# Performance work log

Measured on AMD Instinct MI355X. Metric: run time of the kernel, lower is better.

Reference implementation:

```python
import jax, jax.numpy as jnp
import numpy as np

B, NG, NM, E, K, D = 1, 65536, 8192, 262144, 32, 128
EPS = 1e-5


def layernorm(x, g, b):
    mu = jnp.mean(x, axis=-1, keepdims=True)
    var = jnp.mean(jnp.square(x - mu), axis=-1, keepdims=True)
    return (x - mu) * jax.lax.rsqrt(var + EPS) * g + b


def mlp(x, W, g, b):
    # Linear (no bias) -> tanh -> LayerNorm, matching MLP module
    return layernorm(jnp.tanh(x @ W), g, b)


def setup_inputs() -> dict:
    key = jax.random.key(0)
    ks = jax.random.split(key, 16)
    inp = {
        "grid_mesh_bond_embedding": jax.random.normal(ks[0], (B, E, D), jnp.float32),
        "grid_rect_embedding": jax.random.normal(ks[1], (B, NG, D), jnp.float32),
        "mesh_node_embedding": jax.random.normal(ks[2], (B, NM, D), jnp.float32),
        "edge_id2pair": jnp.stack(
            [jax.random.randint(ks[3], (E,), 0, NG),
             jax.random.randint(ks[4], (E,), 0, NM)], axis=1),  # [E,2] int
        "edge_id_of_node": jax.random.randint(ks[5], (NM, K), 0, E),  # [NM,K] int
        "edge_coef": jax.random.uniform(ks[6], (NM, K, 1), jnp.float32),
        # MLP_G2M_GM2E: Linear(3D -> D), LayerNorm(D)
        "W_gm2e": jax.random.normal(ks[7], (3 * D, D), jnp.float32) / np.sqrt(3 * D),
        "g_gm2e": jnp.ones((D,), jnp.float32),
        "b_gm2e": jnp.zeros((D,), jnp.float32),
        # MLP_G2M_E2M: Linear(2D -> D), LayerNorm(D)
        "W_e2m": jax.random.normal(ks[8], (2 * D, D), jnp.float32) / np.sqrt(2 * D),
        "g_e2m": jnp.ones((D,), jnp.float32),
        "b_e2m": jnp.zeros((D,), jnp.float32),
        # MLP_G2M_G2G: Linear(D -> D), LayerNorm(D)
        "W_g2g": jax.random.normal(ks[9], (D, D), jnp.float32) / np.sqrt(D),
        "g_g2g": jnp.ones((D,), jnp.float32),
        "b_g2g": jnp.zeros((D,), jnp.float32),
    }
    return inp


def reference(grid_mesh_bond_embedding, grid_rect_embedding, mesh_node_embedding,
              edge_id2pair, edge_id_of_node, edge_coef,
              W_gm2e, g_gm2e, b_gm2e, W_e2m, g_e2m, b_e2m, W_g2g, g_g2g, b_g2g):
    # Edge update: gather rect/node endpoints, concat, MLP -> [B,E,D]
    rect_src = grid_rect_embedding[:, edge_id2pair[:, 0]]  # [B,E,D]
    node_dst = mesh_node_embedding[:, edge_id2pair[:, 1]]  # [B,E,D]
    edge_in = jnp.concatenate([grid_mesh_bond_embedding, rect_src, node_dst], axis=-1)
    delta_edge = mlp(edge_in, W_gm2e, g_gm2e, b_gm2e)  # [B,E,D]

    # Node update: gather K edges per mesh node, coef-weighted mean over K
    gathered = delta_edge[:, edge_id_of_node]  # [B,NM,K,D]
    agg = jnp.mean(gathered * edge_coef, axis=-2)  # [B,NM,D]
    delta_node = mlp(jnp.concatenate([mesh_node_embedding, agg], axis=-1), W_e2m, g_e2m, b_e2m)

    # Grid rect self-update
    delta_rect = mlp(grid_rect_embedding, W_g2g, g_g2g, b_g2g)

    return (grid_mesh_bond_embedding + delta_edge,
            grid_rect_embedding + delta_rect,
            mesh_node_embedding + delta_node)
```

## Files before the change

kernel.cpp:

```cpp
#include <hip/hip_runtime.h>


typedef __bf16 bf16x8 __attribute__((ext_vector_type(8)));
typedef __bf16 bf16x4 __attribute__((ext_vector_type(4)));
typedef float f32x4 __attribute__((ext_vector_type(4)));
typedef unsigned int u32x4 __attribute__((ext_vector_type(4)));

#define E_CNT 262144
#define NG_CNT 65536
#define NM_CNT 8192

#define WF_A 0
#define WF_B 16384
#define WF_C 32768
#define WF_3 49152
#define WF_2 65536
#define WF_TOT 98304

__device__ __forceinline__ float fast_tanh(float x) {
  float e = __expf(2.f * x);
  return 1.f - 2.f / (1.f + e);
}

__global__ __launch_bounds__(256) void convert_w_kernel(
    const float* __restrict__ W1, const float* __restrict__ W2,
    const float* __restrict__ W3, __bf16* __restrict__ WF) {
  const int cid = blockIdx.x * 256 + threadIdx.x;
  if (cid >= 12288) return;
  const float* src;
  __bf16* dst;
  int local;
  if (cid < 2048) { src = W1; local = cid; dst = WF + WF_A; }
  else if (cid < 4096) { src = W1 + 128 * 128; local = cid - 2048; dst = WF + WF_B; }
  else if (cid < 6144) { src = W1 + 256 * 128; local = cid - 4096; dst = WF + WF_C; }
  else if (cid < 8192) { src = W3; local = cid - 6144; dst = WF + WF_3; }
  else { src = W2; local = cid - 8192; dst = WF + WF_2; }
  const int lane6 = local & 63, cx = lane6 & 15, qq = lane6 >> 4;
  const int kkn = local >> 6, kk = kkn >> 3, nn = kkn & 7;
  const int k0 = kk * 32 + qq * 8, col = nn * 16 + cx;
  bf16x8 v;
#pragma unroll
  for (int j = 0; j < 8; ++j) v[j] = (__bf16)src[(k0 + j) * 128 + col];
  *(bf16x8*)(dst + local * 8) = v;
}

__device__ __forceinline__ void stage_copy(const __bf16* __restrict__ wf,
                                           __bf16* wt, int nelems) {
  const int n16 = nelems >> 3;
  for (int i = threadIdx.x; i < n16; i += blockDim.x)
    *(u32x4*)(wt + i * 8) = *(const u32x4*)(wf + i * 8);
}

template <bool STORE_D>
__device__ __forceinline__ void mlp_epilogue(f32x4* acc, const f32x4* R,
                                             const float* gvec,
                                             const float* bvec, int q,
                                             float* op, __bf16* dp) {
  float s1 = 0.f, s2 = 0.f;
#pragma unroll
  for (int n = 0; n < 8; ++n)
#pragma unroll
    for (int j = 0; j < 4; ++j) {
      float v = fast_tanh(acc[n][j]);
      acc[n][j] = v;
      s1 += v;
      s2 += v * v;
    }
  s1 += __shfl_xor(s1, 16, 64);
  s2 += __shfl_xor(s2, 16, 64);
  s1 += __shfl_xor(s1, 32, 64);
  s2 += __shfl_xor(s2, 32, 64);
  const float mu = s1 * (1.f / 128.f);
  const float rs = rsqrtf(s2 * (1.f / 128.f) - mu * mu + 1e-5f);
#pragma unroll
  for (int n = 0; n < 8; ++n) {
    const f32x4 G = *(const f32x4*)(gvec + n * 16 + q * 4);
    const f32x4 Bv = *(const f32x4*)(bvec + n * 16 + q * 4);
    f32x4 o;
    bf16x4 db;
#pragma unroll
    for (int j = 0; j < 4; ++j) {
      const float d = (acc[n][j] - mu) * rs * G[j] + Bv[j];
      o[j] = R[n][j] + d;
      db[j] = (__bf16)d;
    }
    *(f32x4*)(op + n * 16 + q * 4) = o;
    if (STORE_D) *(bf16x4*)(dp + n * 16 + q * 4) = db;
  }
}

template <bool STORE_D>
__global__ __launch_bounds__(256, 3) void edge_kernel(
    const float* __restrict__ gm, const int* __restrict__ pair,
    const __bf16* __restrict__ P1, const __bf16* __restrict__ P2,
    const __bf16* __restrict__ WF, const float* __restrict__ gvec,
    const float* __restrict__ bvec, float* __restrict__ out,
    __bf16* __restrict__ delta_out) {
  __shared__ __bf16 wt[16384];
  stage_copy(WF, wt, 16384);
  __syncthreads();
  const int tid = threadIdx.x, lane = tid & 63, wid = tid >> 6;
  const int r = lane & 15, q = lane >> 4;
  const __bf16* wl = wt + lane * 8;
  const int row = ((blockIdx.x * 4 + wid) << 4) + r;

  const int2 sd = *(const int2*)(pair + 2 * (size_t)row);
  const float* pa = gm + (size_t)row * 128;
  f32x4 F[4][2];
#pragma unroll
  for (int kk = 0; kk < 4; ++kk) {
    F[kk][0] = *(const f32x4*)(pa + kk * 32 + q * 8);
    F[kk][1] = *(const f32x4*)(pa + kk * 32 + q * 8 + 4);
  }
  bf16x4 pg1[8], pg2[8];
  {
    const __bf16* p1 = P1 + (size_t)sd.x * 128 + q * 4;
    const __bf16* p2 = P2 + (size_t)sd.y * 128 + q * 4;
#pragma unroll
    for (int n = 0; n < 8; ++n) {
      pg1[n] = *(const bf16x4*)(p1 + n * 16);
      pg2[n] = *(const bf16x4*)(p2 + n * 16);
    }
  }
  f32x4 R[8];
#pragma unroll
  for (int n = 0; n < 8; ++n) R[n] = *(const f32x4*)(pa + n * 16 + q * 4);

  bf16x8 ab[4];
#pragma unroll
  for (int kk = 0; kk < 4; ++kk)
#pragma unroll
    for (int j = 0; j < 4; ++j) {
      ab[kk][j] = (__bf16)F[kk][0][j];
      ab[kk][4 + j] = (__bf16)F[kk][1][j];
    }
  f32x4 acc[8] = {};
#pragma unroll
  for (int kk = 0; kk < 4; ++kk)
#pragma unroll
    for (int n = 0; n < 8; ++n)
      acc[n] = __builtin_amdgcn_mfma_f32_16x16x32_bf16(
          *(const bf16x8*)(wl + (kk * 8 + n) * 512), ab[kk], acc[n], 0, 0, 0);
#pragma unroll
  for (int n = 0; n < 8; ++n)
#pragma unroll
    for (int j = 0; j < 4; ++j)
      acc[n][j] += (float)pg1[n][j] + (float)pg2[n][j];

  mlp_epilogue<STORE_D>(acc, R, gvec, bvec, q, out + (size_t)row * 128,
                        STORE_D ? delta_out + (size_t)row * 128 : nullptr);
}

__global__ __launch_bounds__(256) void rect_fused_kernel(
    const float* __restrict__ rect, const __bf16* __restrict__ WFb,
    const __bf16* __restrict__ WF3, const float* __restrict__ gvec,
    const float* __restrict__ bvec, float* __restrict__ out1,
    __bf16* __restrict__ P1) {
  __shared__ __bf16 wt[32768];
  stage_copy(WFb, wt, 16384);
  stage_copy(WF3, wt + 16384, 16384);
  __syncthreads();
  const int tid = threadIdx.x, lane = tid & 63, wid = tid >> 6;
  const int r = lane & 15, q = lane >> 4;
  const __bf16* wl = wt + lane * 8;
  const int row0 = ((blockIdx.x * 8 + wid) << 4) + r;
#pragma unroll 1
  for (int half = 0; half < 2; ++half) {
    const int row = row0 + half * 64;
    const float* pa = rect + (size_t)row * 128;
    f32x4 F[4][2];
#pragma unroll
    for (int kk = 0; kk < 4; ++kk) {
      F[kk][0] = *(const f32x4*)(pa + kk * 32 + q * 8);
      F[kk][1] = *(const f32x4*)(pa + kk * 32 + q * 8 + 4);
    }
    bf16x8 ab[4];
#pragma unroll
    for (int kk = 0; kk < 4; ++kk)
#pragma unroll
      for (int j = 0; j < 4; ++j) {
        ab[kk][j] = (__bf16)F[kk][0][j];
        ab[kk][4 + j] = (__bf16)F[kk][1][j];
      }
    f32x4 acc[8] = {};
#pragma unroll
    for (int kk = 0; kk < 4; ++kk)
#pragma unroll
      for (int n = 0; n < 8; ++n)
        acc[n] = __builtin_amdgcn_mfma_f32_16x16x32_bf16(
            *(const bf16x8*)(wl + (kk * 8 + n) * 512), ab[kk], acc[n], 0, 0, 0);
    __bf16* pp = P1 + (size_t)row * 128;
#pragma unroll
    for (int n = 0; n < 8; ++n) {
      bf16x4 o;
#pragma unroll
      for (int j = 0; j < 4; ++j) o[j] = (__bf16)acc[n][j];
      *(bf16x4*)(pp + n * 16 + q * 4) = o;
    }
    f32x4 acc2[8] = {};
#pragma unroll
    for (int kk = 0; kk < 4; ++kk)
#pragma unroll
      for (int n = 0; n < 8; ++n)
        acc2[n] = __builtin_amdgcn_mfma_f32_16x16x32_bf16(
            *(const bf16x8*)(wl + 16384 + (kk * 8 + n) * 512), ab[kk], acc2[n],
            0, 0, 0);
    f32x4 R[8];
#pragma unroll
    for (int n = 0; n < 8; ++n) R[n] = *(const f32x4*)(pa + n * 16 + q * 4);
    mlp_epilogue<false>(acc2, R, gvec, bvec, q, out1 + (size_t)row * 128,
                        nullptr);
  }
}

__global__ __launch_bounds__(256) void mlp128_kernel(
    const float* __restrict__ A, const __bf16* __restrict__ WFx,
    const float* __restrict__ gvec, const float* __restrict__ bvec,
    float* __restrict__ out, int M) {
  __shared__ __bf16 wt[16384];
  stage_copy(WFx, wt, 16384);
  __syncthreads();
  const int tid = threadIdx.x, lane = tid & 63, wid = tid >> 6;
  const int r = lane & 15, q = lane >> 4;
  const __bf16* wl = wt + lane * 8;
  const int t = blockIdx.x * 4 + wid;
  if (t >= (M >> 4)) return;
  const int row = (t << 4) + r;
  const float* pa = A + (size_t)row * 128;
  f32x4 F[4][2];
#pragma unroll
  for (int kk = 0; kk < 4; ++kk) {
    F[kk][0] = *(const f32x4*)(pa + kk * 32 + q * 8);
    F[kk][1] = *(const f32x4*)(pa + kk * 32 + q * 8 + 4);
  }
  bf16x8 ab[4];
#pragma unroll
  for (int kk = 0; kk < 4; ++kk)
#pragma unroll
    for (int j = 0; j < 4; ++j) {
      ab[kk][j] = (__bf16)F[kk][0][j];
      ab[kk][4 + j] = (__bf16)F[kk][1][j];
    }
  f32x4 acc[8] = {};
#pragma unroll
  for (int kk = 0; kk < 4; ++kk)
#pragma unroll
    for (int n = 0; n < 8; ++n)
      acc[n] = __builtin_amdgcn_mfma_f32_16x16x32_bf16(
          *(const bf16x8*)(wl + (kk * 8 + n) * 512), ab[kk], acc[n], 0, 0, 0);
  f32x4 R[8];
#pragma unroll
  for (int n = 0; n < 8; ++n) R[n] = *(const f32x4*)(pa + n * 16 + q * 4);
  mlp_epilogue<false>(acc, R, gvec, bvec, q, out + (size_t)row * 128, nullptr);
}

__global__ __launch_bounds__(256) void lin_kernel(
    const float* __restrict__ A, const __bf16* __restrict__ WFx,
    __bf16* __restrict__ out, int M) {
  __shared__ __bf16 wt[16384];
  stage_copy(WFx, wt, 16384);
  __syncthreads();
  const int tid = threadIdx.x, lane = tid & 63, wid = tid >> 6;
  const int r = lane & 15, q = lane >> 4;
  const __bf16* wl = wt + lane * 8;
  const int t = blockIdx.x * 4 + wid;
  if (t >= (M >> 4)) return;
  const int row = (t << 4) + r;
  const float* pa = A + (size_t)row * 128;
  f32x4 F[4][2];
#pragma unroll
  for (int kk = 0; kk < 4; ++kk) {
    F[kk][0] = *(const f32x4*)(pa + kk * 32 + q * 8);
    F[kk][1] = *(const f32x4*)(pa + kk * 32 + q * 8 + 4);
  }
  bf16x8 ab[4];
#pragma unroll
  for (int kk = 0; kk < 4; ++kk)
#pragma unroll
    for (int j = 0; j < 4; ++j) {
      ab[kk][j] = (__bf16)F[kk][0][j];
      ab[kk][4 + j] = (__bf16)F[kk][1][j];
    }
  f32x4 acc[8] = {};
#pragma unroll
  for (int kk = 0; kk < 4; ++kk)
#pragma unroll
    for (int n = 0; n < 8; ++n)
      acc[n] = __builtin_amdgcn_mfma_f32_16x16x32_bf16(
          *(const bf16x8*)(wl + (kk * 8 + n) * 512), ab[kk], acc[n], 0, 0, 0);
  __bf16* po = out + (size_t)row * 128;
#pragma unroll
  for (int n = 0; n < 8; ++n) {
    bf16x4 o;
#pragma unroll
    for (int j = 0; j < 4; ++j) o[j] = (__bf16)acc[n][j];
    *(bf16x4*)(po + n * 16 + q * 4) = o;
  }
}

__global__ __launch_bounds__(256) void node_kernel(
    const __bf16* __restrict__ Ab, const __bf16* __restrict__ WF2,
    const float* __restrict__ gvec, const float* __restrict__ bvec,
    const float* __restrict__ resid, float* __restrict__ out, int M) {
  __shared__ __bf16 wt[32768];
  stage_copy(WF2, wt, 32768);
  __syncthreads();
  const int tid = threadIdx.x, lane = tid & 63, wid = tid >> 6;
  const int r = lane & 15, q = lane >> 4;
  const __bf16* wl = wt + lane * 8;
  const int t = blockIdx.x * 4 + wid;
  if (t >= (M >> 4)) return;
  const int row = (t << 4) + r;
  const __bf16* pb = Ab + (size_t)row * 256 + q * 8;
  bf16x8 ab[8];
#pragma unroll
  for (int kk = 0; kk < 8; ++kk) ab[kk] = *(const bf16x8*)(pb + kk * 32);
  f32x4 R[8];
#pragma unroll
  for (int n = 0; n < 8; ++n)
    R[n] = *(const f32x4*)(resid + (size_t)row * 128 + n * 16 + q * 4);
  f32x4 acc[8] = {};
#pragma unroll
  for (int kk = 0; kk < 8; ++kk)
#pragma unroll
    for (int n = 0; n < 8; ++n)
      acc[n] = __builtin_amdgcn_mfma_f32_16x16x32_bf16(
          *(const bf16x8*)(wl + (kk * 8 + n) * 512), ab[kk], acc[n], 0, 0, 0);
  mlp_epilogue<false>(acc, R, gvec, bvec, q, out + (size_t)row * 128, nullptr);
}

template <bool FROM_WS>
__global__ __launch_bounds__(256) void agg_kernel(
    const __bf16* __restrict__ dws, const float* __restrict__ out0,
    const float* __restrict__ gm, const float* __restrict__ mesh,
    const int* __restrict__ eid, const float* __restrict__ coef,
    __bf16* __restrict__ x2) {
  __shared__ int eid_s[512];
  __shared__ float cf_s[512];
  const int t = threadIdx.x;
  const int n0 = blockIdx.x * 16;
  for (int i = t; i < 512; i += 256) {
    eid_s[i] = eid[n0 * 32 + i];
    cf_s[i] = coef[n0 * 32 + i];
  }
  __syncthreads();
  const int rl = t >> 4;
  const int d8 = (t & 15) * 8;
  const int row = n0 + rl;
  float acc[8] = {0, 0, 0, 0, 0, 0, 0, 0};
  for (int k = 0; k < 32; ++k) {
    const int e = eid_s[rl * 32 + k];
    const float cf = cf_s[rl * 32 + k];
    if (FROM_WS) {
      bf16x8 v = *(const bf16x8*)(dws + (size_t)e * 128 + d8);
#pragma unroll
      for (int j = 0; j < 8; ++j) acc[j] += cf * (float)v[j];
    } else {
      const float* po = out0 + (size_t)e * 128 + d8;
      const float* pg = gm + (size_t)e * 128 + d8;
      f32x4 o0 = *(const f32x4*)po, o1 = *(const f32x4*)(po + 4);
      f32x4 g0 = *(const f32x4*)pg, g1 = *(const f32x4*)(pg + 4);
#pragma unroll
      for (int j = 0; j < 4; ++j) {
        acc[j] += cf * (o0[j] - g0[j]);
        acc[4 + j] += cf * (o1[j] - g1[j]);
      }
    }
  }
  const float* pm = mesh + (size_t)row * 128 + d8;
  f32x4 m0 = *(const f32x4*)pm, m1 = *(const f32x4*)(pm + 4);
  bf16x8 mv, av;
#pragma unroll
  for (int j = 0; j < 4; ++j) {
    mv[j] = (__bf16)m0[j];
    mv[4 + j] = (__bf16)m1[j];
  }
#pragma unroll
  for (int j = 0; j < 8; ++j) av[j] = (__bf16)(acc[j] * (1.0f / 32.0f));
  *(bf16x8*)(x2 + (size_t)row * 256 + d8) = mv;
  *(bf16x8*)(x2 + (size_t)row * 256 + 128 + d8) = av;
}

extern "C" void kernel_launch(void* const* d_in, const int* in_sizes, int n_in,
                              void* d_out, int out_size, void* d_ws,
                              size_t ws_size, hipStream_t stream) {
  const float* gm = (const float*)d_in[0];
  const float* rect = (const float*)d_in[1];
  const float* mesh = (const float*)d_in[2];
  const int* pair = (const int*)d_in[3];
  const int* eid = (const int*)d_in[4];
  const float* coef = (const float*)d_in[5];
  const float* W1 = (const float*)d_in[6];
  const float* g1 = (const float*)d_in[7];
  const float* b1 = (const float*)d_in[8];
  const float* W2 = (const float*)d_in[9];
  const float* g2 = (const float*)d_in[10];
  const float* b2 = (const float*)d_in[11];
  const float* W3 = (const float*)d_in[12];
  const float* g3 = (const float*)d_in[13];
  const float* b3 = (const float*)d_in[14];

  float* out0 = (float*)d_out;
  float* out1 = out0 + (size_t)E_CNT * 128;
  float* out2 = out1 + (size_t)NG_CNT * 128;

  const size_t wfBytes = (size_t)WF_TOT * 2;
  const size_t wfoff = (ws_size - wfBytes) & ~(size_t)63;
  __bf16* WF = (__bf16*)((char*)d_ws + wfoff);

  const size_t deltaE = (size_t)E_CNT * 128;
  const size_t x2E = (size_t)NM_CNT * 256;
  const size_t p1E = (size_t)NG_CNT * 128;
  const bool fastD = wfoff >= (deltaE + x2E) * 2;
  const bool fastP = wfoff >= (deltaE + x2E + p1E) * 2;

  __bf16* delta = (__bf16*)d_ws;
  __bf16* x2 = fastD ? delta + deltaE : (__bf16*)d_ws;
  __bf16* P1ws = delta + deltaE + x2E;
  __bf16* P2 = (__bf16*)out2;

  convert_w_kernel<<<48, 256, 0, stream>>>(W1, W2, W3, WF);

  const __bf16* P1;
  if (fastP) {
    rect_fused_kernel<<<512, 256, 0, stream>>>(rect, WF + WF_B, WF + WF_3, g3,
                                               b3, out1, P1ws);
    P1 = P1ws;
  } else {
    lin_kernel<<<1024, 256, 0, stream>>>(rect, WF + WF_B, (__bf16*)out1,
                                         NG_CNT);
    P1 = (const __bf16*)out1;
  }
  lin_kernel<<<128, 256, 0, stream>>>(mesh, WF + WF_C, P2, NM_CNT);

  if (fastD) {
    edge_kernel<true><<<4096, 256, 0, stream>>>(gm, pair, P1, P2, WF + WF_A,
                                                g1, b1, out0, delta);
    agg_kernel<true><<<512, 256, 0, stream>>>(delta, nullptr, nullptr, mesh,
                                              eid, coef, x2);
  } else {
    edge_kernel<false><<<4096, 256, 0, stream>>>(gm, pair, P1, P2, WF + WF_A,
                                                 g1, b1, out0, nullptr);
    agg_kernel<false><<<512, 256, 0, stream>>>(nullptr, out0, gm, mesh, eid,
                                               coef, x2);
  }
  if (!fastP) {
    mlp128_kernel<<<1024, 256, 0, stream>>>(rect, WF + WF_3, g3, b3, out1,
                                            NG_CNT);
  }
  node_kernel<<<128, 256, 0, stream>>>(x2, WF + WF_2, g2, b2, mesh, out2,
                                       NM_CNT);
}
```

Before: 204.7 us.

## Read MFMA weights directly from global memory instead of staging in LDS

Removes the per-block LDS staging of pre-swizzled bf16 weight fragments (and the __syncthreads) in all GEMM kernels, so each lane reads its weight fragments straight from global/L2. Output stores in the MLP epilogues become nontemporal to avoid polluting cache. The rect kernel now handles one 64-row tile per block with twice the grid, the edge kernel drops its occupancy hint, and the aggregation loop is unrolled. Global weight reads rely on cache hits and may add latency compared with LDS, in exchange for lower LDS use, higher occupancy, and no block-start copy.

```diff
diff --git a/kernel.cpp b/kernel.cpp
--- a/kernel.cpp
+++ b/kernel.cpp
@@ -4,7 +4,6 @@
 typedef __bf16 bf16x8 __attribute__((ext_vector_type(8)));
 typedef __bf16 bf16x4 __attribute__((ext_vector_type(4)));
 typedef float f32x4 __attribute__((ext_vector_type(4)));
-typedef unsigned int u32x4 __attribute__((ext_vector_type(4)));
 
 #define E_CNT 262144
 #define NG_CNT 65536
@@ -44,14 +43,7 @@
   *(bf16x8*)(dst + local * 8) = v;
 }
 
-__device__ __forceinline__ void stage_copy(const __bf16* __restrict__ wf,
-                                           __bf16* wt, int nelems) {
-  const int n16 = nelems >> 3;
-  for (int i = threadIdx.x; i < n16; i += blockDim.x)
-    *(u32x4*)(wt + i * 8) = *(const u32x4*)(wf + i * 8);
-}
-
-template <bool STORE_D>
+template <bool STORE_D, bool NT>
 __device__ __forceinline__ void mlp_epilogue(f32x4* acc, const f32x4* R,
                                              const float* gvec,
                                              const float* bvec, int q,
@@ -84,24 +76,24 @@
       o[j] = R[n][j] + d;
       db[j] = (__bf16)d;
     }
-    *(f32x4*)(op + n * 16 + q * 4) = o;
+    if (NT)
+      __builtin_nontemporal_store(o, (f32x4*)(op + n * 16 + q * 4));
+    else
+      *(f32x4*)(op + n * 16 + q * 4) = o;
     if (STORE_D) *(bf16x4*)(dp + n * 16 + q * 4) = db;
   }
 }
 
 template <bool STORE_D>
-__global__ __launch_bounds__(256, 3) void edge_kernel(
+__global__ __launch_bounds__(256) void edge_kernel(
     const float* __restrict__ gm, const int* __restrict__ pair,
     const __bf16* __restrict__ P1, const __bf16* __restrict__ P2,
     const __bf16* __restrict__ WF, const float* __restrict__ gvec,
     const float* __restrict__ bvec, float* __restrict__ out,
     __bf16* __restrict__ delta_out) {
-  __shared__ __bf16 wt[16384];
-  stage_copy(WF, wt, 16384);
-  __syncthreads();
   const int tid = threadIdx.x, lane = tid & 63, wid = tid >> 6;
   const int r = lane & 15, q = lane >> 4;
-  const __bf16* wl = wt + lane * 8;
+  const __bf16* wl = WF + lane * 8;
   const int row = ((blockIdx.x * 4 + wid) << 4) + r;
 
   const int2 sd = *(const int2*)(pair + 2 * (size_t)row);
@@ -147,8 +139,8 @@
     for (int j = 0; j < 4; ++j)
       acc[n][j] += (float)pg1[n][j] + (float)pg2[n][j];
 
-  mlp_epilogue<STORE_D>(acc, R, gvec, bvec, q, out + (size_t)row * 128,
-                        STORE_D ? delta_out + (size_t)row * 128 : nullptr);
+  mlp_epilogue<STORE_D, true>(acc, R, gvec, bvec, q, out + (size_t)row * 128,
+                              STORE_D ? delta_out + (size_t)row * 128 : nullptr);
 }
 
 __global__ __launch_bounds__(256) void rect_fused_kernel(
@@ -156,73 +148,62 @@
     const __bf16* __restrict__ WF3, const float* __restrict__ gvec,
     const float* __restrict__ bvec, float* __restrict__ out1,
     __bf16* __restrict__ P1) {
-  __shared__ __bf16 wt[32768];
-  stage_copy(WFb, wt, 16384);
-  stage_copy(WF3, wt + 16384, 16384);
-  __syncthreads();
   const int tid = threadIdx.x, lane = tid & 63, wid = tid >> 6;
   const int r = lane & 15, q = lane >> 4;
-  const __bf16* wl = wt + lane * 8;
-  const int row0 = ((blockIdx.x * 8 + wid) << 4) + r;
-#pragma unroll 1
-  for (int half = 0; half < 2; ++half) {
-    const int row = row0 + half * 64;
-    const float* pa = rect + (size_t)row * 128;
-    f32x4 F[4][2];
-#pragma unroll
-    for (int kk = 0; kk < 4; ++kk) {
-      F[kk][0] = *(const f32x4*)(pa + kk * 32 + q * 8);
-      F[kk][1] = *(const f32x4*)(pa + kk * 32 + q * 8 + 4);
-    }
-    bf16x8 ab[4];
-#pragma unroll
-    for (int kk = 0; kk < 4; ++kk)
-#pragma unroll
-      for (int j = 0; j < 4; ++j) {
-        ab[kk][j] = (__bf16)F[kk][0][j];
-        ab[kk][4 + j] = (__bf16)F[kk][1][j];
-      }
-    f32x4 acc[8] = {};
-#pragma unroll
-    for (int kk = 0; kk < 4; ++kk)
-#pragma unroll
-      for (int n = 0; n < 8; ++n)
-        acc[n] = __builtin_amdgcn_mfma_f32_16x16x32_bf16(
-            *(const bf16x8*)(wl + (kk * 8 + n) * 512), ab[kk], acc[n], 0, 0, 0);
-    __bf16* pp = P1 + (size_t)row * 128;
-#pragma unroll
-    for (int n = 0; n < 8; ++n) {
-      bf16x4 o;
-#pragma unroll
-      for (int j = 0; j < 4; ++j) o[j] = (__bf16)acc[n][j];
-      *(bf16x4*)(pp + n * 16 + q * 4) = o;
-    }
-    f32x4 acc2[8] = {};
-#pragma unroll
-    for (int kk = 0; kk < 4; ++kk)
-#pragma unroll
-      for (int n = 0; n < 8; ++n)
-        acc2[n] = __builtin_amdgcn_mfma_f32_16x16x32_bf16(
-            *(const bf16x8*)(wl + 16384 + (kk * 8 + n) * 512), ab[kk], acc2[n],
-            0, 0, 0);
-    f32x4 R[8];
-#pragma unroll
-    for (int n = 0; n < 8; ++n) R[n] = *(const f32x4*)(pa + n * 16 + q * 4);
-    mlp_epilogue<false>(acc2, R, gvec, bvec, q, out1 + (size_t)row * 128,
-                        nullptr);
-  }
+  const __bf16* wlb = WFb + lane * 8;
+  const __bf16* wl3 = WF3 + lane * 8;
+  const int row = ((blockIdx.x * 4 + wid) << 4) + r;
+  const float* pa = rect + (size_t)row * 128;
+  f32x4 F[4][2];
+#pragma unroll
+  for (int kk = 0; kk < 4; ++kk) {
+    F[kk][0] = *(const f32x4*)(pa + kk * 32 + q * 8);
+    F[kk][1] = *(const f32x4*)(pa + kk * 32 + q * 8 + 4);
+  }
+  f32x4 R[8];
+#pragma unroll
+  for (int n = 0; n < 8; ++n) R[n] = *(const f32x4*)(pa + n * 16 + q * 4);
+  bf16x8 ab[4];
+#pragma unroll
+  for (int kk = 0; kk < 4; ++kk)
+#pragma unroll
+    for (int j = 0; j < 4; ++j) {
+      ab[kk][j] = (__bf16)F[kk][0][j];
+      ab[kk][4 + j] = (__bf16)F[kk][1][j];
+    }
+  f32x4 acc[8] = {};
+#pragma unroll
+  for (int kk = 0; kk < 4; ++kk)
+#pragma unroll
+    for (int n = 0; n < 8; ++n)
+      acc[n] = __builtin_amdgcn_mfma_f32_16x16x32_bf16(
+          *(const bf16x8*)(wlb + (kk * 8 + n) * 512), ab[kk], acc[n], 0, 0, 0);
+  __bf16* pp = P1 + (size_t)row * 128;
+#pragma unroll
+  for (int n = 0; n < 8; ++n) {
+    bf16x4 o;
+#pragma unroll
+    for (int j = 0; j < 4; ++j) o[j] = (__bf16)acc[n][j];
+    *(bf16x4*)(pp + n * 16 + q * 4) = o;
+  }
+  f32x4 acc2[8] = {};
+#pragma unroll
+  for (int kk = 0; kk < 4; ++kk)
+#pragma unroll
+    for (int n = 0; n < 8; ++n)
+      acc2[n] = __builtin_amdgcn_mfma_f32_16x16x32_bf16(
+          *(const bf16x8*)(wl3 + (kk * 8 + n) * 512), ab[kk], acc2[n], 0, 0, 0);
+  mlp_epilogue<false, true>(acc2, R, gvec, bvec, q, out1 + (size_t)row * 128,
+                            nullptr);
 }
 
 __global__ __launch_bounds__(256) void mlp128_kernel(
     const float* __restrict__ A, const __bf16* __restrict__ WFx,
     const float* __restrict__ gvec, const float* __restrict__ bvec,
     float* __restrict__ out, int M) {
-  __shared__ __bf16 wt[16384];
-  stage_copy(WFx, wt, 16384);
-  __syncthreads();
   const int tid = threadIdx.x, lane = tid & 63, wid = tid >> 6;
   const int r = lane & 15, q = lane >> 4;
-  const __bf16* wl = wt + lane * 8;
+  const __bf16* wl = WFx + lane * 8;
   const int t = blockIdx.x * 4 + wid;
   if (t >= (M >> 4)) return;
   const int row = (t << 4) + r;
@@ -251,18 +232,16 @@
   f32x4 R[8];
 #pragma unroll
   for (int n = 0; n < 8; ++n) R[n] = *(const f32x4*)(pa + n * 16 + q * 4);
-  mlp_epilogue<false>(acc, R, gvec, bvec, q, out + (size_t)row * 128, nullptr);
+  mlp_epilogue<false, true>(acc, R, gvec, bvec, q, out + (size_t)row * 128,
+                            nullptr);
 }
 
 __global__ __launch_bounds__(256) void lin_kernel(
     const float* __restrict__ A, const __bf16* __restrict__ WFx,
     __bf16* __restrict__ out, int M) {
-  __shared__ __bf16 wt[16384];
-  stage_copy(WFx, wt, 16384);
-  __syncthreads();
   const int tid = threadIdx.x, lane = tid & 63, wid = tid >> 6;
   const int r = lane & 15, q = lane >> 4;
-  const __bf16* wl = wt + lane * 8;
+  const __bf16* wl = WFx + lane * 8;
   const int t = blockIdx.x * 4 + wid;
   if (t >= (M >> 4)) return;
   const int row = (t << 4) + r;
@@ -302,12 +281,9 @@
     const __bf16* __restrict__ Ab, const __bf16* __restrict__ WF2,
     const float* __restrict__ gvec, const float* __restrict__ bvec,
     const float* __restrict__ resid, float* __restrict__ out, int M) {
-  __shared__ __bf16 wt[32768];
-  stage_copy(WF2, wt, 32768);
-  __syncthreads();
   const int tid = threadIdx.x, lane = tid & 63, wid = tid >> 6;
   const int r = lane & 15, q = lane >> 4;
-  const __bf16* wl = wt + lane * 8;
+  const __bf16* wl = WF2 + lane * 8;
   const int t = blockIdx.x * 4 + wid;
   if (t >= (M >> 4)) return;
   const int row = (t << 4) + r;
@@ -326,7 +302,8 @@
     for (int n = 0; n < 8; ++n)
       acc[n] = __builtin_amdgcn_mfma_f32_16x16x32_bf16(
           *(const bf16x8*)(wl + (kk * 8 + n) * 512), ab[kk], acc[n], 0, 0, 0);
-  mlp_epilogue<false>(acc, R, gvec, bvec, q, out + (size_t)row * 128, nullptr);
+  mlp_epilogue<false, true>(acc, R, gvec, bvec, q, out + (size_t)row * 128,
+                            nullptr);
 }
 
 template <bool FROM_WS>
@@ -348,6 +325,7 @@
   const int d8 = (t & 15) * 8;
   const int row = n0 + rl;
   float acc[8] = {0, 0, 0, 0, 0, 0, 0, 0};
+#pragma unroll 8
   for (int k = 0; k < 32; ++k) {
     const int e = eid_s[rl * 32 + k];
     const float cf = cf_s[rl * 32 + k];
@@ -423,8 +401,8 @@
 
   const __bf16* P1;
   if (fastP) {
-    rect_fused_kernel<<<512, 256, 0, stream>>>(rect, WF + WF_B, WF + WF_3, g3,
-                                               b3, out1, P1ws);
+    rect_fused_kernel<<<1024, 256, 0, stream>>>(rect, WF + WF_B, WF + WF_3, g3,
+                                                b3, out1, P1ws);
     P1 = P1ws;
   } else {
     lin_kernel<<<1024, 256, 0, stream>>>(rect, WF + WF_B, (__bf16*)out1,
```

Result: faster. 185.2 us (-9.5%).
